# Performance work log

Measured on AMD Instinct MI355X. Metric: run time of the kernel, lower is better.

Reference implementation:

```python
import jax, jax.numpy as jnp
import numpy as np

N_NODES = 10000
N_EDGES = 640000
D = 128
BN_EPS = 1e-5


def setup_inputs() -> dict:
    key = jax.random.key(0)
    k1, k2, k3 = jax.random.split(key, 3)
    x = jax.random.normal(k1, (N_NODES, D), dtype=jnp.float32)
    edge_index = jax.random.randint(k2, (2, N_EDGES), 0, N_NODES, dtype=jnp.int64)
    W = jax.random.normal(k3, (D, D), dtype=jnp.float32) * (1.0 / np.sqrt(D))
    b = jnp.zeros((D,), dtype=jnp.float32)
    gamma = jnp.ones((D,), dtype=jnp.float32)
    beta = jnp.zeros((D,), dtype=jnp.float32)
    return {"x": x, "edge_index": edge_index, "W": W, "b": b, "gamma": gamma, "beta": beta}


def reference(x, edge_index, W, b, gamma, beta):
    # GINConv: out_i = MLP((1+eps)*x_i + sum_{j->i} x_j), eps=0
    src = edge_index[0]
    dst = edge_index[1]
    agg = jax.ops.segment_sum(x[src], dst, num_segments=N_NODES)  # [N, D]
    h = agg + x  # (1 + eps) * x with eps = 0
    # MLP inside GINConv: Linear + ReLU
    h = jnp.maximum(h @ W + b, 0.0)
    # outer F.relu (idempotent after inner ReLU, kept for faithfulness)
    h = jnp.maximum(h, 0.0)
    # BatchNorm1d, training-mode batch statistics (biased variance)
    mean = jnp.mean(h, axis=0)
    var = jnp.var(h, axis=0)
    h = (h - mean) * jax.lax.rsqrt(var + BN_EPS) * gamma + beta
    # Dropout in eval mode -> identity. his_x = [h]; return the main output.
    return h
```

## Files before the change

### kernel.cpp

```cpp
#include <hip/hip_runtime.h>

#define N_NODES 10000
#define N_EDGES 640000
#define D 128
#define BN_EPS 1e-5f
#define CAP 128
#define NSTRIPE 16
#define RPB 8
#define NB 313
#define BCAP 2400
#define ABLK 128
#define ASLICE 5000
#define CSENT 319

typedef _Float16 half4_t __attribute__((ext_vector_type(4)));
typedef unsigned short u16;

__global__ __launch_bounds__(256) void k_bin(
    const int* __restrict__ ei,
    const float4* __restrict__ x4,
    int* cur,
    int* __restrict__ recs,
    half4_t* __restrict__ xh)
{
    __shared__ int cnt[NB];
    __shared__ int base[NB];
    const int b = blockIdx.x, t = threadIdx.x;

    {
        const int n4 = N_NODES * D / 4;
        for (int i = b * 256 + t; i < n4; i += ABLK * 256) {
            const float4 v = x4[i];
            half4_t h;
            h.x = (_Float16)v.x; h.y = (_Float16)v.y;
            h.z = (_Float16)v.z; h.w = (_Float16)v.w;
            xh[i] = h;
        }
    }

    for (int i = t; i < NB; i += 256) cnt[i] = 0;
    __syncthreads();

    const int e0 = b * ASLICE;
    for (int i = t; i < ASLICE; i += 256)
        atomicAdd(&cnt[ei[N_EDGES + e0 + i] >> 5], 1);
    __syncthreads();

    const unsigned cbase = (unsigned)cur[CSENT];
    for (int i = t; i < NB; i += 256) {
        const int c = cnt[i];
        base[i] = (int)((unsigned)atomicAdd(&cur[i], c) - cbase);
        cnt[i] = 0;
    }
    __syncthreads();

    for (int i = t; i < ASLICE; i += 256) {
        const int e = e0 + i;
        const int d = ei[N_EDGES + e];
        const int s = ei[e];
        const int bin = d >> 5;
        const int p = base[bin] + atomicAdd(&cnt[bin], 1);
        if (p < BCAP) recs[bin * BCAP + p] = (s << 5) | (d & 31);
    }
}

__global__ __launch_bounds__(256) void k_gfill(
    const float* __restrict__ x,
    const half4_t* __restrict__ xh4,
    const int* __restrict__ cur,
    const int* __restrict__ recs,
    const float* __restrict__ W,
    const float* __restrict__ bias,
    float* __restrict__ out,
    float* __restrict__ stats)
{
    __shared__ u16 lst[RPB * CAP];
    __shared__ int cnt[RPB];
    __shared__ float hs[RPB][D];
    const int tid  = threadIdx.x;
    const int bin  = blockIdx.x >> 2;
    const int q    = blockIdx.x & 3;
    const int wv   = tid >> 6;
    const int lane = tid & 63;
    const int h    = lane >> 5;
    const int l    = lane & 31;
    const float4* __restrict__ x4 = (const float4*)x;

    if (tid < RPB) cnt[tid] = 0;
    __syncthreads();

    const unsigned cbase = (unsigned)cur[CSENT];
    int nrec = (int)((unsigned)cur[bin] - cbase);
    if (nrec > BCAP) nrec = BCAP;
    const int* __restrict__ br = recs + bin * BCAP;
    for (int i = tid; i < nrec; i += 256) {
        const int r = br[i];
        const int dl = r & 31;
        if ((dl >> 3) == q) {
            const int p = atomicAdd(&cnt[dl & 7], 1);
            if (p < CAP) lst[(dl & 7) * CAP + p] = (u16)(r >> 5);
        }
    }
    __syncthreads();

    #pragma unroll
    for (int j = 0; j < 2; j++) {
        const int lrow = wv * 2 + j;
        const int node = blockIdx.x * RPB + lrow;
        int n = cnt[lrow];
        if (n > CAP) n = CAP;
        const u16* __restrict__ myl = &lst[lrow * CAP];
        float4 acc = make_float4(0.f, 0.f, 0.f, 0.f);
        int i = 0;
        for (; i + 64 <= n; i += 64) {
            const int sj = (int)myl[i + lane];
            #pragma unroll
            for (int b = 0; b < 2; b++) {
                half4_t v[16];
                #pragma unroll
                for (int u = 0; u < 16; u++) {
                    const int p = b * 16 + u;
                    const int s = __shfl(sj, 2 * p + h, 64);
                    v[u] = xh4[(size_t)s * 32 + l];
                }
                #pragma unroll
                for (int u = 0; u < 16; u++) {
                    acc.x += (float)v[u].x; acc.y += (float)v[u].y;
                    acc.z += (float)v[u].z; acc.w += (float)v[u].w;
                }
            }
        }
        const int c = n - i;
        if (c > 0) {
            const int sj = (lane < c) ? (int)myl[i + lane] : 0;
            const int pairs = c >> 1;
            for (int t2 = 0; t2 < pairs; t2 += 16) {
                half4_t v[16];
                #pragma unroll
                for (int u = 0; u < 16; u++) {
                    const int s = __shfl(sj, (2 * (t2 + u) + h) & 63, 64);
                    v[u] = xh4[(size_t)s * 32 + l];
                }
                #pragma unroll
                for (int u = 0; u < 16; u++) {
                    if (t2 + u < pairs) {
                        acc.x += (float)v[u].x; acc.y += (float)v[u].y;
                        acc.z += (float)v[u].z; acc.w += (float)v[u].w;
                    }
                }
            }
            if (c & 1) {
                const int s = __shfl(sj, c - 1, 64);
                const half4_t vv = xh4[(size_t)s * 32 + l];
                if (h == 0) {
                    acc.x += (float)vv.x; acc.y += (float)vv.y;
                    acc.z += (float)vv.z; acc.w += (float)vv.w;
                }
            }
        }
        acc.x += __shfl_xor(acc.x, 32, 64);
        acc.y += __shfl_xor(acc.y, 32, 64);
        acc.z += __shfl_xor(acc.z, 32, 64);
        acc.w += __shfl_xor(acc.w, 32, 64);
        if (h == 0) {
            const float4 xv = x4[(size_t)node * 32 + l];
            float4 o;
            o.x = acc.x + xv.x; o.y = acc.y + xv.y;
            o.z = acc.z + xv.z; o.w = acc.w + xv.w;
            *(float4*)&hs[lrow][4 * l] = o;
        }
    }
    __syncthreads();

    const int col = tid & 127;
    const int rg  = tid >> 7;
    float a[4] = {0.f, 0.f, 0.f, 0.f};
    #pragma unroll 8
    for (int k = 0; k < D; k++) {
        const float w = W[k * D + col];
        #pragma unroll
        for (int r = 0; r < 4; r++)
            a[r] = fmaf(hs[rg * 4 + r][k], w, a[r]);
    }

    const float bcol = bias[col];
    float s1 = 0.f, s2 = 0.f;
    #pragma unroll
    for (int r = 0; r < 4; r++) {
        const float v = fmaxf(a[r] + bcol, 0.f);
        out[(size_t)(blockIdx.x * RPB + rg * 4 + r) * D + col] = v;
        s1 += v;
        s2 += v * v;
    }

    __syncthreads();
    float* red = &hs[0][0];
    red[tid]       = s1;
    red[256 + tid] = s2;
    __syncthreads();
    if (tid < D) {
        float* sp = &stats[(size_t)(blockIdx.x & (NSTRIPE - 1)) * 256];
        atomicAdd(&sp[tid],     red[tid]       + red[tid + 128]);
        atomicAdd(&sp[D + tid], red[256 + tid] + red[256 + tid + 128]);
    }
}

__global__ __launch_bounds__(256) void k_bn(
    float* out,
    const float* __restrict__ stats,
    const float* __restrict__ gamma,
    const float* __restrict__ beta)
{
    __shared__ float sc[D], sh[D];
    const int tid = threadIdx.x;
    if (tid < D) {
        const float fbase = stats[NSTRIPE * 256];
        float s = 0.f, q = 0.f;
        #pragma unroll
        for (int cp = 0; cp < NSTRIPE; cp++) {
            s += stats[cp * 256 + tid]     - fbase;
            q += stats[cp * 256 + D + tid] - fbase;
        }
        const float mean = s * (1.0f / N_NODES);
        const float var  = q * (1.0f / N_NODES) - mean * mean;
        const float scale = gamma[tid] * rsqrtf(var + BN_EPS);
        sc[tid] = scale;
        sh[tid] = beta[tid] - mean * scale;
    }
    __syncthreads();

    float4* o4 = (float4*)out;
    #pragma unroll
    for (int j = 0; j < 2; j++) {
        const int f = blockIdx.x * 512 + j * 256 + tid;
        const int c = (f & 31) << 2;
        float4 v = o4[f];
        v.x = v.x * sc[c]     + sh[c];
        v.y = v.y * sc[c + 1] + sh[c + 1];
        v.z = v.z * sc[c + 2] + sh[c + 2];
        v.w = v.w * sc[c + 3] + sh[c + 3];
        o4[f] = v;
    }
}

extern "C" void kernel_launch(void* const* d_in, const int* in_sizes, int n_in,
                              void* d_out, int out_size, void* d_ws, size_t ws_size,
                              hipStream_t stream)
{
    const float* x     = (const float*)d_in[0];
    const int*   ei    = (const int*)d_in[1];
    const float* W     = (const float*)d_in[2];
    const float* bias  = (const float*)d_in[3];
    const float* gamma = (const float*)d_in[4];
    const float* beta  = (const float*)d_in[5];
    float* out = (float*)d_out;

    float*   stats = (float*)d_ws;
    int*     cur   = (int*)(stats + NSTRIPE * 256 + 8);
    int*     recs  = cur + 320;
    half4_t* xh    = (half4_t*)(recs + NB * BCAP);

    k_bin<<<ABLK, 256, 0, stream>>>(ei, (const float4*)x, cur, recs, xh);
    k_gfill<<<N_NODES / RPB, 256, 0, stream>>>(x, xh, cur, recs, W, bias, out, stats);
    k_bn<<<N_NODES * D / 2048, 256, 0, stream>>>(out, stats, gamma, beta);
}
```

Baseline: 122.6 us.

## Bin edges per 8-node block and gather fp16 rows with 16-byte loads

```diff
diff --git a/kernel.cpp b/kernel.cpp
--- a/kernel.cpp
+++ b/kernel.cpp
@@ -7,13 +7,13 @@
 #define CAP 128
 #define NSTRIPE 16
 #define RPB 8
-#define NB 313
-#define BCAP 2400
+#define NB 1250
+#define BCAP 704
 #define ABLK 128
 #define ASLICE 5000
-#define CSENT 319
-
-typedef _Float16 half4_t __attribute__((ext_vector_type(4)));
+#define CSENT 1250
+
+typedef _Float16 half8_t __attribute__((ext_vector_type(8)));
 typedef unsigned short u16;
 
 __global__ __launch_bounds__(256) void k_bin(
@@ -21,19 +21,22 @@
     const float4* __restrict__ x4,
     int* cur,
     int* __restrict__ recs,
-    half4_t* __restrict__ xh)
+    half8_t* __restrict__ xh)
 {
     __shared__ int cnt[NB];
     __shared__ int base[NB];
     const int b = blockIdx.x, t = threadIdx.x;
 
     {
-        const int n4 = N_NODES * D / 4;
-        for (int i = b * 256 + t; i < n4; i += ABLK * 256) {
-            const float4 v = x4[i];
-            half4_t h;
-            h.x = (_Float16)v.x; h.y = (_Float16)v.y;
-            h.z = (_Float16)v.z; h.w = (_Float16)v.w;
+        const int n8 = N_NODES * D / 8;
+        for (int i = b * 256 + t; i < n8; i += ABLK * 256) {
+            const float4 a = x4[2 * i];
+            const float4 c = x4[2 * i + 1];
+            half8_t h;
+            h[0] = (_Float16)a.x; h[1] = (_Float16)a.y;
+            h[2] = (_Float16)a.z; h[3] = (_Float16)a.w;
+            h[4] = (_Float16)c.x; h[5] = (_Float16)c.y;
+            h[6] = (_Float16)c.z; h[7] = (_Float16)c.w;
             xh[i] = h;
         }
     }
@@ -43,7 +46,7 @@
 
     const int e0 = b * ASLICE;
     for (int i = t; i < ASLICE; i += 256)
-        atomicAdd(&cnt[ei[N_EDGES + e0 + i] >> 5], 1);
+        atomicAdd(&cnt[ei[N_EDGES + e0 + i] >> 3], 1);
     __syncthreads();
 
     const unsigned cbase = (unsigned)cur[CSENT];
@@ -58,15 +61,15 @@
         const int e = e0 + i;
         const int d = ei[N_EDGES + e];
         const int s = ei[e];
-        const int bin = d >> 5;
+        const int bin = d >> 3;
         const int p = base[bin] + atomicAdd(&cnt[bin], 1);
-        if (p < BCAP) recs[bin * BCAP + p] = (s << 5) | (d & 31);
+        if (p < BCAP) recs[bin * BCAP + p] = (s << 3) | (d & 7);
     }
 }
 
 __global__ __launch_bounds__(256) void k_gfill(
     const float* __restrict__ x,
-    const half4_t* __restrict__ xh4,
+    const half8_t* __restrict__ xh8,
     const int* __restrict__ cur,
     const int* __restrict__ recs,
     const float* __restrict__ W,
@@ -78,12 +81,11 @@
     __shared__ int cnt[RPB];
     __shared__ float hs[RPB][D];
     const int tid  = threadIdx.x;
-    const int bin  = blockIdx.x >> 2;
-    const int q    = blockIdx.x & 3;
+    const int bin  = blockIdx.x;
     const int wv   = tid >> 6;
     const int lane = tid & 63;
-    const int h    = lane >> 5;
-    const int l    = lane & 31;
+    const int qq   = lane >> 4;
+    const int l    = lane & 15;
     const float4* __restrict__ x4 = (const float4*)x;
 
     if (tid < RPB) cnt[tid] = 0;
@@ -95,79 +97,83 @@
     const int* __restrict__ br = recs + bin * BCAP;
     for (int i = tid; i < nrec; i += 256) {
         const int r = br[i];
-        const int dl = r & 31;
-        if ((dl >> 3) == q) {
-            const int p = atomicAdd(&cnt[dl & 7], 1);
-            if (p < CAP) lst[(dl & 7) * CAP + p] = (u16)(r >> 5);
-        }
+        const int p = atomicAdd(&cnt[r & 7], 1);
+        if (p < CAP) lst[(r & 7) * CAP + p] = (u16)(r >> 3);
     }
     __syncthreads();
 
     #pragma unroll
     for (int j = 0; j < 2; j++) {
         const int lrow = wv * 2 + j;
-        const int node = blockIdx.x * RPB + lrow;
+        const int node = bin * RPB + lrow;
         int n = cnt[lrow];
         if (n > CAP) n = CAP;
         const u16* __restrict__ myl = &lst[lrow * CAP];
-        float4 acc = make_float4(0.f, 0.f, 0.f, 0.f);
+        float acc[8];
+        #pragma unroll
+        for (int z = 0; z < 8; z++) acc[z] = 0.f;
+
         int i = 0;
         for (; i + 64 <= n; i += 64) {
             const int sj = (int)myl[i + lane];
             #pragma unroll
             for (int b = 0; b < 2; b++) {
-                half4_t v[16];
-                #pragma unroll
-                for (int u = 0; u < 16; u++) {
-                    const int p = b * 16 + u;
-                    const int s = __shfl(sj, 2 * p + h, 64);
-                    v[u] = xh4[(size_t)s * 32 + l];
-                }
-                #pragma unroll
-                for (int u = 0; u < 16; u++) {
-                    acc.x += (float)v[u].x; acc.y += (float)v[u].y;
-                    acc.z += (float)v[u].z; acc.w += (float)v[u].w;
-                }
+                half8_t v[8];
+                #pragma unroll
+                for (int u = 0; u < 8; u++) {
+                    const int s = __shfl(sj, 4 * (b * 8 + u) + qq, 64);
+                    v[u] = xh8[(size_t)s * 16 + l];
+                }
+                #pragma unroll
+                for (int u = 0; u < 8; u++)
+                    #pragma unroll
+                    for (int z = 0; z < 8; z++)
+                        acc[z] += (float)v[u][z];
             }
         }
         const int c = n - i;
         if (c > 0) {
             const int sj = (lane < c) ? (int)myl[i + lane] : 0;
-            const int pairs = c >> 1;
-            for (int t2 = 0; t2 < pairs; t2 += 16) {
-                half4_t v[16];
-                #pragma unroll
-                for (int u = 0; u < 16; u++) {
-                    const int s = __shfl(sj, (2 * (t2 + u) + h) & 63, 64);
-                    v[u] = xh4[(size_t)s * 32 + l];
-                }
-                #pragma unroll
-                for (int u = 0; u < 16; u++) {
-                    if (t2 + u < pairs) {
-                        acc.x += (float)v[u].x; acc.y += (float)v[u].y;
-                        acc.z += (float)v[u].z; acc.w += (float)v[u].w;
+            const int quads = c >> 2;
+            for (int t2 = 0; t2 < quads; t2 += 8) {
+                half8_t v[8];
+                #pragma unroll
+                for (int u = 0; u < 8; u++) {
+                    const int s = __shfl(sj, (4 * (t2 + u) + qq) & 63, 64);
+                    v[u] = xh8[(size_t)s * 16 + l];
+                }
+                #pragma unroll
+                for (int u = 0; u < 8; u++) {
+                    if (t2 + u < quads) {
+                        #pragma unroll
+                        for (int z = 0; z < 8; z++)
+                            acc[z] += (float)v[u][z];
                     }
                 }
             }
-            if (c & 1) {
-                const int s = __shfl(sj, c - 1, 64);
-                const half4_t vv = xh4[(size_t)s * 32 + l];
-                if (h == 0) {
-                    acc.x += (float)vv.x; acc.y += (float)vv.y;
-                    acc.z += (float)vv.z; acc.w += (float)vv.w;
+            const int r = c & 3;
+            if (r > 0) {
+                const int s = __shfl(sj, (4 * quads + qq) & 63, 64);
+                const half8_t vv = xh8[(size_t)s * 16 + l];
+                if (qq < r) {
+                    #pragma unroll
+                    for (int z = 0; z < 8; z++)
+                        acc[z] += (float)vv[z];
                 }
             }
         }
-        acc.x += __shfl_xor(acc.x, 32, 64);
-        acc.y += __shfl_xor(acc.y, 32, 64);
-        acc.z += __shfl_xor(acc.z, 32, 64);
-        acc.w += __shfl_xor(acc.w, 32, 64);
-        if (h == 0) {
-            const float4 xv = x4[(size_t)node * 32 + l];
-            float4 o;
-            o.x = acc.x + xv.x; o.y = acc.y + xv.y;
-            o.z = acc.z + xv.z; o.w = acc.w + xv.w;
-            *(float4*)&hs[lrow][4 * l] = o;
+        #pragma unroll
+        for (int z = 0; z < 8; z++) {
+            acc[z] += __shfl_xor(acc[z], 16, 64);
+            acc[z] += __shfl_xor(acc[z], 32, 64);
+        }
+        if (qq == 0) {
+            const float4 xa = x4[(size_t)node * 32 + 2 * l];
+            const float4 xb = x4[(size_t)node * 32 + 2 * l + 1];
+            *(float4*)&hs[lrow][8 * l] =
+                make_float4(acc[0] + xa.x, acc[1] + xa.y, acc[2] + xa.z, acc[3] + xa.w);
+            *(float4*)&hs[lrow][8 * l + 4] =
+                make_float4(acc[4] + xb.x, acc[5] + xb.y, acc[6] + xb.z, acc[7] + xb.w);
         }
     }
     __syncthreads();
@@ -188,7 +194,7 @@
     #pragma unroll
     for (int r = 0; r < 4; r++) {
         const float v = fmaxf(a[r] + bcol, 0.f);
-        out[(size_t)(blockIdx.x * RPB + rg * 4 + r) * D + col] = v;
+        out[(size_t)(bin * RPB + rg * 4 + r) * D + col] = v;
         s1 += v;
         s2 += v * v;
     }
@@ -199,7 +205,7 @@
     red[256 + tid] = s2;
     __syncthreads();
     if (tid < D) {
-        float* sp = &stats[(size_t)(blockIdx.x & (NSTRIPE - 1)) * 256];
+        float* sp = &stats[(size_t)(bin & (NSTRIPE - 1)) * 256];
         atomicAdd(&sp[tid],     red[tid]       + red[tid + 128]);
         atomicAdd(&sp[D + tid], red[256 + tid] + red[256 + tid + 128]);
     }
@@ -257,10 +263,10 @@
 
     float*   stats = (float*)d_ws;
     int*     cur   = (int*)(stats + NSTRIPE * 256 + 8);
-    int*     recs  = cur + 320;
-    half4_t* xh    = (half4_t*)(recs + NB * BCAP);
+    int*     recs  = cur + 1280;
+    half8_t* xh    = (half8_t*)(recs + NB * BCAP);
 
     k_bin<<<ABLK, 256, 0, stream>>>(ei, (const float4*)x, cur, recs, xh);
-    k_gfill<<<N_NODES / RPB, 256, 0, stream>>>(x, xh, cur, recs, W, bias, out, stats);
+    k_gfill<<<NB, 256, 0, stream>>>(x, xh, cur, recs, W, bias, out, stats);
     k_bn<<<N_NODES * D / 2048, 256, 0, stream>>>(out, stats, gamma, beta);
 }
```

New measurement: 118.6 us. 1.03x faster.
